# Performance work log

Hardware: AMD Instinct MI355X
Metric: run time of the kernel (lower is better)

Reference implementation:

```python
import jax, jax.numpy as jnp
import numpy as np

EPS = 1e-8

def squash(t, axis=-1):
    sq = jnp.sum(t * t, axis=axis, keepdims=True)
    scale = sq / (1.0 + sq)
    return scale * t / jnp.sqrt(sq + EPS)

def setup_inputs() -> dict:
    key = jax.random.key(0)
    k1, k2 = jax.random.split(key)
    B, N_IN, D_IN, N_OUT, D_OUT = 256, 1152, 8, 10, 16
    x = jax.random.normal(k1, (B, N_IN, D_IN), dtype=jnp.float32)
    W = 0.01 * jax.random.normal(k2, (1, N_IN, N_OUT, D_OUT, D_IN), dtype=jnp.float32)
    return {"x": x, "W": W}

def reference(x, W):
    # u_hat[b,n,o,j] = sum_i W[0,n,o,j,i] * x[b,n,i]   -> (B, N_in, N_out, D_out)
    u_hat = jnp.einsum('noji,bni->bnoj', W[0], x)
    # b_ij starts with batch dim 1 (as in original torch code) and broadcasts
    b_ij = jnp.zeros((1, u_hat.shape[1], u_hat.shape[2], 1), dtype=u_hat.dtype)
    v_j = None
    for _ in range(3):  # fixed 3 routing iterations
        c_ij = jax.nn.softmax(b_ij, axis=2)            # over output capsules
        s_j = jnp.sum(c_ij * u_hat, axis=1, keepdims=True)  # (B,1,N_out,D_out)
        v_j = squash(s_j, axis=-1)
        b_ij = b_ij + jnp.sum(u_hat * v_j, axis=-1, keepdims=True)
    return jnp.squeeze(v_j, axis=1)  # (B, N_out, D_out)
```

## Files before the change

### kernel.cpp

```cpp
#include <hip/hip_runtime.h>

#define B_ 256
#define N_IN 1152
#define N_OUT 10
#define D_OUT 16
#define OJ 160
#define SN (B_*OJ)
#define LOG2E 1.44269504088896340736f
#define NPB 16
#define NPW 4
#define NGB (N_IN/NPB)

typedef __attribute__((ext_vector_type(8))) short bf16x8;
typedef __attribute__((ext_vector_type(4))) float f32x4;

#define NW_ELEMS (N_IN*N_OUT*D_OUT)
#define NWB (NW_ELEMS/256)
#define XTB ((N_IN/16)*(B_/16))

__device__ __forceinline__ unsigned short f2bf(float f) {
  unsigned u = __float_as_uint(f);
  u += 0x7fffu + ((u >> 16) & 1u);
  return (unsigned short)(u >> 16);
}
__device__ __forceinline__ float bf2f(unsigned short s) {
  return __uint_as_float(((unsigned)s) << 16);
}

template<int CTRL>
__device__ __forceinline__ float dpp_add(float x) {
  int y = __builtin_amdgcn_mov_dpp(__float_as_int(x), CTRL, 0xF, 0xF, false);
  return x + __int_as_float(y);
}
__device__ __forceinline__ float row_sum16(float x) {
  x = dpp_add<0x128>(x); x = dpp_add<0x124>(x);
  x = dpp_add<0x122>(x); x = dpp_add<0x121>(x);
  return x;
}

__global__ __launch_bounds__(256) void pack_all(const float* __restrict__ W,
                                                const float* __restrict__ x,
                                                short* __restrict__ WH, short* __restrict__ WL,
                                                short* __restrict__ XH, short* __restrict__ XL) {
  const int bid = blockIdx.x;
  const int tid = threadIdx.x;
  if (bid < NWB) {
    const int t = bid*256 + tid;
    const float4 a = ((const float4*)W)[t*2];
    const float4 b = ((const float4*)W)[t*2+1];
    const float w[8] = {a.x,a.y,a.z,a.w,b.x,b.y,b.z,b.w};
    bf16x8 vh, vl;
#pragma unroll
    for (int e=0;e<8;e++){
      unsigned short hh = f2bf(w[e]);
      vh[e] = (short)hh;
      vl[e] = (short)f2bf(w[e] - bf2f(hh));
    }
    ((bf16x8*)WH)[t] = vh;
    ((bf16x8*)WL)[t] = vl;
  } else {
    __shared__ bf16x8 TH[16*17], TL[16*17];
    const int bid2 = bid - NWB;
    const int nt = bid2 >> 4, bt = bid2 & 15;
    const int nn = tid & 15, bb = tid >> 4;
    const size_t r = (size_t)((bt*16 + bb)*N_IN + nt*16 + nn);
    const float4 a = ((const float4*)x)[r*2];
    const float4 c = ((const float4*)x)[r*2+1];
    const float w[8] = {a.x,a.y,a.z,a.w,c.x,c.y,c.z,c.w};
    bf16x8 vh, vl;
#pragma unroll
    for (int e=0;e<8;e++){
      unsigned short hh = f2bf(w[e]);
      vh[e] = (short)hh;
      vl[e] = (short)f2bf(w[e] - bf2f(hh));
    }
    TH[nn*17 + bb] = vh;
    TL[nn*17 + bb] = vl;
    __syncthreads();
    const int bb2 = tid & 15, nn2 = tid >> 4;
    const size_t o = (size_t)(nt*16 + nn2)*B_ + bt*16 + bb2;
    ((bf16x8*)XH)[o] = TH[nn2*17 + bb2];
    ((bf16x8*)XL)[o] = TL[nn2*17 + bb2];
  }
}


__global__ __launch_bounds__(256) void pass1(const short* __restrict__ WH,
                                             const short* __restrict__ WL,
                                             const short* __restrict__ XH,
                                             const short* __restrict__ XL,
                                             float* __restrict__ P) {
  __shared__ f32x4 red[3*640];
  const int tid = threadIdx.x, w = tid >> 6, l = tid & 63;
  const int bb = l & 15, c = l >> 4;
  const int b0 = blockIdx.y * 16;
  const int n0 = blockIdx.x * NPB + w * NPW;
  const short* Abase = (c & 1)  ? WL : WH;
  const short* Bbase = (c >> 1) ? XL : XH;

  f32x4 acc[N_OUT];
  const f32x4 zz = {0.f,0.f,0.f,0.f};
#pragma unroll
  for (int o=0;o<N_OUT;o++) acc[o] = zz;

  for (int nn=0; nn<NPW; ++nn) {
    const int n = n0 + nn;
    const bf16x8 bfrag = *(const bf16x8*)&Bbase[((size_t)n*B_ + b0 + bb)*8];
    const short* Ap = &Abase[(size_t)n*1280 + bb*8];
#pragma unroll
    for (int o=0;o<N_OUT;o++) {
      const bf16x8 afrag = *(const bf16x8*)&Ap[o*128];
      acc[o] = __builtin_amdgcn_mfma_f32_16x16x32_bf16(afrag, bfrag, acc[o], 0,0,0);
    }
  }

  const int slot = bb*4 + c;
  if (w) {
    f32x4* r = &red[(w-1)*640];
#pragma unroll
    for (int o=0;o<N_OUT;o++) r[o*64 + slot] = acc[o];
  }
  __syncthreads();
  if (!w) {
#pragma unroll
    for (int o=0;o<N_OUT;o++)
      acc[o] += red[o*64+slot] + red[640+o*64+slot] + red[1280+o*64+slot];
    float* Pp = &P[((size_t)blockIdx.x*B_ + b0 + bb)*OJ + c*4];
#pragma unroll
    for (int o=0;o<N_OUT;o++) *(f32x4*)&Pp[o*16] = acc[o];
  }
}

__global__ __launch_bounds__(256) void pass23(const short* __restrict__ WH,
                                              const short* __restrict__ WL,
                                              const short* __restrict__ XH,
                                              const short* __restrict__ XL,
                                              const float* __restrict__ veff,
                                              float* __restrict__ P) {
  __shared__ f32x4 red[3*640];
  const int tid = threadIdx.x, w = tid >> 6, l = tid & 63;
  const int bb = l & 15, c = l >> 4;
  const int b0 = blockIdx.y * 16;
  const int n0 = blockIdx.x * NPB + w * NPW;
  const short* Abase = (c & 1)  ? WL : WH;
  const short* Bbase = (c >> 1) ? XL : XH;

  f32x4 vj[N_OUT], acc[N_OUT];
  const f32x4 zz = {0.f,0.f,0.f,0.f};
  const float* vp = &veff[(size_t)(b0+bb)*OJ + c*4];
#pragma unroll
  for (int o=0;o<N_OUT;o++) { vj[o] = *(const f32x4*)&vp[o*16]; acc[o] = zz; }

  for (int nn=0; nn<NPW; ++nn) {
    const int n = n0 + nn;
    const bf16x8 bfrag = *(const bf16x8*)&Bbase[((size_t)n*B_ + b0 + bb)*8];
    const short* Ap = &Abase[(size_t)n*1280 + bb*8];
    f32x4 u[N_OUT];
#pragma unroll
    for (int o=0;o<N_OUT;o++) {
      const bf16x8 afrag = *(const bf16x8*)&Ap[o*128];
      u[o] = __builtin_amdgcn_mfma_f32_16x16x32_bf16(afrag, bfrag, zz, 0,0,0);
    }
    float ez[N_OUT], Z = 0.f;
#pragma unroll
    for (int o=0;o<N_OUT;o++) {
      float t = u[o][0]*vj[o][0] + u[o][1]*vj[o][1]
              + u[o][2]*vj[o][2] + u[o][3]*vj[o][3];
      t += __shfl_xor(t, 16);
      t += __shfl_xor(t, 32);
      ez[o] = exp2f(t);
      Z += ez[o];
    }
    const float invZ = 1.f / Z;
#pragma unroll
    for (int o=0;o<N_OUT;o++) acc[o] += (ez[o] * invZ) * u[o];
  }

  const int slot = bb*4 + c;
  if (w) {
    f32x4* r = &red[(w-1)*640];
#pragma unroll
    for (int o=0;o<N_OUT;o++) r[o*64 + slot] = acc[o];
  }
  __syncthreads();
  if (!w) {
#pragma unroll
    for (int o=0;o<N_OUT;o++)
      acc[o] += red[o*64+slot] + red[640+o*64+slot] + red[1280+o*64+slot];
    float* Pp = &P[((size_t)blockIdx.x*B_ + b0 + bb)*OJ + c*4];
#pragma unroll
    for (int o=0;o<N_OUT;o++) *(f32x4*)&Pp[o*16] = acc[o];
  }
}

__global__ __launch_bounds__(256) void finish(const float* __restrict__ P, float scale,
                                              const float* __restrict__ vprev,
                                              float* __restrict__ vout, float lscale) {
  const int idx = blockIdx.x*256 + threadIdx.x;
  float t = 0.f;
#pragma unroll 8
  for (int g=0; g<NGB; ++g) t += P[(size_t)g*SN + idx];
  t *= scale;
  const float sq = row_sum16(t * t);
  float v = t * (sq / (1.f + sq)) * rsqrtf(sq + 1e-8f);
  v *= lscale;
  if (vprev != nullptr) v += vprev[idx];
  vout[idx] = v;
}

extern "C" void kernel_launch(void* const* d_in, const int* in_sizes, int n_in,
                              void* d_out, int out_size, void* d_ws, size_t ws_size,
                              hipStream_t stream) {
  const float* x = (const float*)d_in[0];
  const float* W = (const float*)d_in[1];
  float* out = (float*)d_out;

  float* P   = (float*)d_ws;
  float* v1  = P  + (size_t)NGB*SN;
  float* v12 = v1 + SN;
  short* WH = (short*)(v12 + SN);
  short* WL = WH + (size_t)NW_ELEMS*8;
  short* XH = WL + (size_t)NW_ELEMS*8;
  short* XL = XH + (size_t)(B_*N_IN)*8;

  pack_all<<<NWB + XTB, 256, 0, stream>>>(W, x, WH, WL, XH, XL);

  const dim3 pg(NGB, 16), pb(256);

  pass1<<<pg, pb, 0, stream>>>(WH, WL, XH, XL, P);
  finish<<<SN/256, 256, 0, stream>>>(P, 0.1f, nullptr, v1, LOG2E);

  pass23<<<pg, pb, 0, stream>>>(WH, WL, XH, XL, v1, P);
  finish<<<SN/256, 256, 0, stream>>>(P, 1.0f, v1, v12, LOG2E);

  pass23<<<pg, pb, 0, stream>>>(WH, WL, XH, XL, v12, P);
  finish<<<SN/256, 256, 0, stream>>>(P, 1.0f, nullptr, out, 1.0f);
}
```

Before: 88.59 us.

## Fuse packing and routing passes into a single cooperative persistent kernel

Replaces seven separate launches (pack, three passes, three finishes) with one cooperative kernel of 256 blocks × 512 threads that uses grid.sync between stages, removing launch gaps. The n-split drops from 72 groups to 16, so each block covers 72 n values with 8 waves and a tree reduction in LDS, and the finish step reads 16 partials instead of 72. A fallback launches the old multi-kernel path if the cooperative launch fails. Risks: grid-wide barrier cost, only 256 blocks for the packing stage, and less parallelism per pass.

```diff
diff --git a/kernel.cpp b/kernel.cpp
--- a/kernel.cpp
+++ b/kernel.cpp
@@ -1,22 +1,25 @@
 #include <hip/hip_runtime.h>
+#include <hip/hip_cooperative_groups.h>
+
+namespace cg = cooperative_groups;
 
 #define B_ 256
 #define N_IN 1152
 #define N_OUT 10
-#define D_OUT 16
 #define OJ 160
 #define SN (B_*OJ)
 #define LOG2E 1.44269504088896340736f
-#define NPB 16
-#define NPW 4
-#define NGB (N_IN/NPB)
+#define SGN 16
+#define NPS (N_IN/SGN)
+#define NTHR 512
+#define NBLK 256
+#define GSZ (NBLK*NTHR)
+#define NW_ELEMS (N_IN*N_OUT*16)
+#define NX_ELEMS (B_*N_IN)
+#define NTILES ((N_IN/16)*(B_/16))
 
 typedef __attribute__((ext_vector_type(8))) short bf16x8;
 typedef __attribute__((ext_vector_type(4))) float f32x4;
-
-#define NW_ELEMS (N_IN*N_OUT*D_OUT)
-#define NWB (NW_ELEMS/256)
-#define XTB ((N_IN/16)*(B_/16))
 
 __device__ __forceinline__ unsigned short f2bf(float f) {
   unsigned u = __float_as_uint(f);
@@ -26,94 +29,281 @@
 __device__ __forceinline__ float bf2f(unsigned short s) {
   return __uint_as_float(((unsigned)s) << 16);
 }
+__device__ __forceinline__ void split8(const float* p, bf16x8& vh, bf16x8& vl) {
+  const float4 a = *(const float4*)p;
+  const float4 b = *(const float4*)(p + 4);
+  const float w[8] = {a.x,a.y,a.z,a.w,b.x,b.y,b.z,b.w};
+#pragma unroll
+  for (int e=0;e<8;e++){
+    unsigned short hh = f2bf(w[e]);
+    vh[e] = (short)hh;
+    vl[e] = (short)f2bf(w[e] - bf2f(hh));
+  }
+}
 
 template<int CTRL>
-__device__ __forceinline__ float dpp_add(float x) {
-  int y = __builtin_amdgcn_mov_dpp(__float_as_int(x), CTRL, 0xF, 0xF, false);
-  return x + __int_as_float(y);
-}
-__device__ __forceinline__ float row_sum16(float x) {
-  x = dpp_add<0x128>(x); x = dpp_add<0x124>(x);
-  x = dpp_add<0x122>(x); x = dpp_add<0x121>(x);
-  return x;
-}
-
-__global__ __launch_bounds__(256) void pack_all(const float* __restrict__ W,
-                                                const float* __restrict__ x,
-                                                short* __restrict__ WH, short* __restrict__ WL,
-                                                short* __restrict__ XH, short* __restrict__ XL) {
+__device__ __forceinline__ float dpp_add(float xx) {
+  int y = __builtin_amdgcn_mov_dpp(__float_as_int(xx), CTRL, 0xF, 0xF, false);
+  return xx + __int_as_float(y);
+}
+__device__ __forceinline__ float row_sum16(float xx) {
+  xx = dpp_add<0x128>(xx); xx = dpp_add<0x124>(xx);
+  xx = dpp_add<0x122>(xx); xx = dpp_add<0x121>(xx);
+  return xx;
+}
+__device__ __forceinline__ float squash_elem(float t) {
+  const float sq = row_sum16(t * t);
+  return t * (sq / (1.f + sq)) * rsqrtf(sq + 1e-8f);
+}
+
+template<bool UNIFORM>
+__device__ __forceinline__ void pass_core(const short* __restrict__ Abase,
+                                          const short* __restrict__ Bbase,
+                                          const float* __restrict__ veff,
+                                          float* __restrict__ P,
+                                          float (*red)[2560],
+                                          int sg, int b0, int n0,
+                                          int w, int bb, int c) {
+  const f32x4 zz = {0.f,0.f,0.f,0.f};
+  f32x4 acc[N_OUT], vj[N_OUT];
+#pragma unroll
+  for (int o=0;o<N_OUT;o++) acc[o] = zz;
+  if (!UNIFORM) {
+    const float* vp = &veff[(size_t)(b0+bb)*OJ + c*4];
+#pragma unroll
+    for (int o=0;o<N_OUT;o++) vj[o] = *(const f32x4*)&vp[o*16];
+  }
+  for (int k=0;k<9;k++) {
+    const int n = n0 + w + 8*k;
+    const bf16x8 bfrag = *(const bf16x8*)&Bbase[((size_t)n*B_ + b0 + bb)*8];
+    const short* Ap = &Abase[(size_t)n*1280 + bb*8];
+    if (UNIFORM) {
+#pragma unroll
+      for (int o=0;o<N_OUT;o++) {
+        const bf16x8 afrag = *(const bf16x8*)&Ap[o*128];
+        acc[o] = __builtin_amdgcn_mfma_f32_16x16x32_bf16(afrag, bfrag, acc[o], 0,0,0);
+      }
+    } else {
+      f32x4 u[N_OUT];
+#pragma unroll
+      for (int o=0;o<N_OUT;o++) {
+        const bf16x8 afrag = *(const bf16x8*)&Ap[o*128];
+        u[o] = __builtin_amdgcn_mfma_f32_16x16x32_bf16(afrag, bfrag, zz, 0,0,0);
+      }
+      float ez[N_OUT], Z = 0.f;
+#pragma unroll
+      for (int o=0;o<N_OUT;o++) {
+        float t = u[o][0]*vj[o][0] + u[o][1]*vj[o][1]
+                + u[o][2]*vj[o][2] + u[o][3]*vj[o][3];
+        t += __shfl_xor(t, 16);
+        t += __shfl_xor(t, 32);
+        ez[o] = exp2f(t);
+        Z += ez[o];
+      }
+      const float invZ = 1.f / Z;
+#pragma unroll
+      for (int o=0;o<N_OUT;o++) acc[o] += (ez[o]*invZ) * u[o];
+    }
+  }
+  const int slot4 = (bb*4 + c)*4;
+  if (w >= 4) {
+#pragma unroll
+    for (int o=0;o<N_OUT;o++) *(f32x4*)&red[w-4][o*256 + slot4] = acc[o];
+  }
+  __syncthreads();
+  if (w < 4) {
+#pragma unroll
+    for (int o=0;o<N_OUT;o++) acc[o] += *(const f32x4*)&red[w][o*256 + slot4];
+  }
+  __syncthreads();
+  if (w == 2 || w == 3) {
+#pragma unroll
+    for (int o=0;o<N_OUT;o++) *(f32x4*)&red[w-2][o*256 + slot4] = acc[o];
+  }
+  __syncthreads();
+  if (w < 2) {
+#pragma unroll
+    for (int o=0;o<N_OUT;o++) acc[o] += *(const f32x4*)&red[w][o*256 + slot4];
+  }
+  __syncthreads();
+  if (w == 1) {
+#pragma unroll
+    for (int o=0;o<N_OUT;o++) *(f32x4*)&red[0][o*256 + slot4] = acc[o];
+  }
+  __syncthreads();
+  if (w == 0) {
+    float* Pp = &P[(size_t)sg*SN + (size_t)(b0+bb)*OJ + c*4];
+#pragma unroll
+    for (int o=0;o<N_OUT;o++) {
+      acc[o] += *(const f32x4*)&red[0][o*256 + slot4];
+      *(f32x4*)&Pp[o*16] = acc[o];
+    }
+  }
+  __syncthreads();
+}
+
+__global__ __launch_bounds__(NTHR) void caps_mega(
+    const float* __restrict__ W, const float* __restrict__ x,
+    short* __restrict__ WH, short* __restrict__ WL,
+    short* __restrict__ XH, short* __restrict__ XL,
+    float* __restrict__ P, float* __restrict__ v1buf,
+    float* __restrict__ v12buf, float* __restrict__ out) {
+  cg::grid_group grid = cg::this_grid();
+  __shared__ float red[4][2560];
+  const int tid = threadIdx.x;
   const int bid = blockIdx.x;
-  const int tid = threadIdx.x;
+  const int gtid = bid*NTHR + tid;
+
+  for (int t = gtid; t < NW_ELEMS; t += GSZ) {
+    bf16x8 vh, vl;
+    split8(W + (size_t)t*8, vh, vl);
+    ((bf16x8*)WH)[t] = vh; ((bf16x8*)WL)[t] = vl;
+  }
+  {
+    const int unit = tid >> 8, utid = tid & 255;
+    bf16x8* TH = (bf16x8*)red + unit*544;
+    bf16x8* TL = TH + 272;
+    for (int iter = 0; iter < 3; ++iter) {
+      const int tile = iter*(NBLK*2) + bid*2 + unit;
+      const bool ok = tile < NTILES;
+      int nt = 0, bt = 0;
+      if (ok) {
+        nt = tile >> 4; bt = tile & 15;
+        const int nn = utid & 15, bb = utid >> 4;
+        bf16x8 vh, vl;
+        split8(x + ((size_t)(bt*16+bb)*N_IN + nt*16+nn)*8, vh, vl);
+        TH[nn*17 + bb] = vh; TL[nn*17 + bb] = vl;
+      }
+      __syncthreads();
+      if (ok) {
+        const int bb2 = utid & 15, nn2 = utid >> 4;
+        const size_t o = (size_t)(nt*16+nn2)*B_ + bt*16 + bb2;
+        ((bf16x8*)XH)[o] = TH[nn2*17 + bb2];
+        ((bf16x8*)XL)[o] = TL[nn2*17 + bb2];
+      }
+      __syncthreads();
+    }
+  }
+  grid.sync();
+
+  const int sg = bid >> 4, bg = bid & 15;
+  const int b0 = bg*16, n0 = sg*NPS;
+  const int w = tid >> 6, l = tid & 63;
+  const int bb = l & 15, c = l >> 4;
+  const short* Abase = (c & 1)  ? WL : WH;
+  const short* Bbase = (c >> 1) ? XL : XH;
+
+  pass_core<true>(Abase, Bbase, nullptr, P, red, sg, b0, n0, w, bb, c);
+  grid.sync();
+  if (gtid < SN) {
+    float s = 0.f;
+#pragma unroll
+    for (int g=0; g<SGN; ++g) s += P[(size_t)g*SN + gtid];
+    v1buf[gtid] = squash_elem(0.1f*s) * LOG2E;
+  }
+  grid.sync();
+  pass_core<false>(Abase, Bbase, v1buf, P, red, sg, b0, n0, w, bb, c);
+  grid.sync();
+  if (gtid < SN) {
+    float s = 0.f;
+#pragma unroll
+    for (int g=0; g<SGN; ++g) s += P[(size_t)g*SN + gtid];
+    v12buf[gtid] = v1buf[gtid] + squash_elem(s) * LOG2E;
+  }
+  grid.sync();
+  pass_core<false>(Abase, Bbase, v12buf, P, red, sg, b0, n0, w, bb, c);
+  grid.sync();
+  if (gtid < SN) {
+    float s = 0.f;
+#pragma unroll
+    for (int g=0; g<SGN; ++g) s += P[(size_t)g*SN + gtid];
+    out[gtid] = squash_elem(s);
+  }
+}
+
+#define NWB (NW_ELEMS/256)
+__global__ __launch_bounds__(256) void fb_pack(const float* __restrict__ W,
+                                               const float* __restrict__ x,
+                                               short* __restrict__ WH, short* __restrict__ WL,
+                                               short* __restrict__ XH, short* __restrict__ XL) {
+  const int bid = blockIdx.x, tid = threadIdx.x;
   if (bid < NWB) {
     const int t = bid*256 + tid;
-    const float4 a = ((const float4*)W)[t*2];
-    const float4 b = ((const float4*)W)[t*2+1];
-    const float w[8] = {a.x,a.y,a.z,a.w,b.x,b.y,b.z,b.w};
-    bf16x8 vh, vl;
-#pragma unroll
-    for (int e=0;e<8;e++){
-      unsigned short hh = f2bf(w[e]);
-      vh[e] = (short)hh;
-      vl[e] = (short)f2bf(w[e] - bf2f(hh));
-    }
-    ((bf16x8*)WH)[t] = vh;
-    ((bf16x8*)WL)[t] = vl;
+    bf16x8 vh, vl; split8(W + (size_t)t*8, vh, vl);
+    ((bf16x8*)WH)[t] = vh; ((bf16x8*)WL)[t] = vl;
   } else {
     __shared__ bf16x8 TH[16*17], TL[16*17];
-    const int bid2 = bid - NWB;
-    const int nt = bid2 >> 4, bt = bid2 & 15;
+    const int tile = bid - NWB;
+    const int nt = tile >> 4, bt = tile & 15;
     const int nn = tid & 15, bb = tid >> 4;
-    const size_t r = (size_t)((bt*16 + bb)*N_IN + nt*16 + nn);
-    const float4 a = ((const float4*)x)[r*2];
-    const float4 c = ((const float4*)x)[r*2+1];
-    const float w[8] = {a.x,a.y,a.z,a.w,c.x,c.y,c.z,c.w};
     bf16x8 vh, vl;
-#pragma unroll
-    for (int e=0;e<8;e++){
-      unsigned short hh = f2bf(w[e]);
-      vh[e] = (short)hh;
-      vl[e] = (short)f2bf(w[e] - bf2f(hh));
-    }
-    TH[nn*17 + bb] = vh;
-    TL[nn*17 + bb] = vl;
+    split8(x + ((size_t)(bt*16+bb)*N_IN + nt*16+nn)*8, vh, vl);
+    TH[nn*17 + bb] = vh; TL[nn*17 + bb] = vl;
     __syncthreads();
     const int bb2 = tid & 15, nn2 = tid >> 4;
-    const size_t o = (size_t)(nt*16 + nn2)*B_ + bt*16 + bb2;
+    const size_t o = (size_t)(nt*16+nn2)*B_ + bt*16 + bb2;
     ((bf16x8*)XH)[o] = TH[nn2*17 + bb2];
     ((bf16x8*)XL)[o] = TL[nn2*17 + bb2];
   }
 }
 
-
-__global__ __launch_bounds__(256) void pass1(const short* __restrict__ WH,
-                                             const short* __restrict__ WL,
-                                             const short* __restrict__ XH,
-                                             const short* __restrict__ XL,
-                                             float* __restrict__ P) {
+template<bool UNIFORM>
+__global__ __launch_bounds__(256) void fb_pass(const short* __restrict__ WH,
+                                               const short* __restrict__ WL,
+                                               const short* __restrict__ XH,
+                                               const short* __restrict__ XL,
+                                               const float* __restrict__ veff,
+                                               float* __restrict__ P) {
   __shared__ f32x4 red[3*640];
   const int tid = threadIdx.x, w = tid >> 6, l = tid & 63;
   const int bb = l & 15, c = l >> 4;
-  const int b0 = blockIdx.y * 16;
-  const int n0 = blockIdx.x * NPB + w * NPW;
+  const int sg = blockIdx.x, bg = blockIdx.y;
+  const int b0 = bg*16;
+  const int n0 = sg*NPS + w*18;
   const short* Abase = (c & 1)  ? WL : WH;
   const short* Bbase = (c >> 1) ? XL : XH;
 
-  f32x4 acc[N_OUT];
   const f32x4 zz = {0.f,0.f,0.f,0.f};
+  f32x4 acc[N_OUT], vj[N_OUT];
 #pragma unroll
   for (int o=0;o<N_OUT;o++) acc[o] = zz;
-
-  for (int nn=0; nn<NPW; ++nn) {
+  if (!UNIFORM) {
+    const float* vp = &veff[(size_t)(b0+bb)*OJ + c*4];
+#pragma unroll
+    for (int o=0;o<N_OUT;o++) vj[o] = *(const f32x4*)&vp[o*16];
+  }
+  for (int nn=0; nn<18; ++nn) {
     const int n = n0 + nn;
     const bf16x8 bfrag = *(const bf16x8*)&Bbase[((size_t)n*B_ + b0 + bb)*8];
     const short* Ap = &Abase[(size_t)n*1280 + bb*8];
-#pragma unroll
-    for (int o=0;o<N_OUT;o++) {
-      const bf16x8 afrag = *(const bf16x8*)&Ap[o*128];
-      acc[o] = __builtin_amdgcn_mfma_f32_16x16x32_bf16(afrag, bfrag, acc[o], 0,0,0);
+    if (UNIFORM) {
+#pragma unroll
+      for (int o=0;o<N_OUT;o++) {
+        const bf16x8 afrag = *(const bf16x8*)&Ap[o*128];
+        acc[o] = __builtin_amdgcn_mfma_f32_16x16x32_bf16(afrag, bfrag, acc[o], 0,0,0);
+      }
+    } else {
+      f32x4 u[N_OUT];
+#pragma unroll
+      for (int o=0;o<N_OUT;o++) {
+        const bf16x8 afrag = *(const bf16x8*)&Ap[o*128];
+        u[o] = __builtin_amdgcn_mfma_f32_16x16x32_bf16(afrag, bfrag, zz, 0,0,0);
+      }
+      float ez[N_OUT], Z = 0.f;
+#pragma unroll
+      for (int o=0;o<N_OUT;o++) {
+        float t = u[o][0]*vj[o][0] + u[o][1]*vj[o][1]
+                + u[o][2]*vj[o][2] + u[o][3]*vj[o][3];
+        t += __shfl_xor(t, 16);
+        t += __shfl_xor(t, 32);
+        ez[o] = exp2f(t);
+        Z += ez[o];
+      }
+      const float invZ = 1.f / Z;
+#pragma unroll
+      for (int o=0;o<N_OUT;o++) acc[o] += (ez[o]*invZ)*u[o];
     }
   }
-
   const int slot = bb*4 + c;
   if (w) {
     f32x4* r = &red[(w-1)*640];
@@ -125,85 +315,21 @@
 #pragma unroll
     for (int o=0;o<N_OUT;o++)
       acc[o] += red[o*64+slot] + red[640+o*64+slot] + red[1280+o*64+slot];
-    float* Pp = &P[((size_t)blockIdx.x*B_ + b0 + bb)*OJ + c*4];
+    float* Pp = &P[(size_t)sg*SN + (size_t)(b0+bb)*OJ + c*4];
 #pragma unroll
     for (int o=0;o<N_OUT;o++) *(f32x4*)&Pp[o*16] = acc[o];
   }
 }
 
-__global__ __launch_bounds__(256) void pass23(const short* __restrict__ WH,
-                                              const short* __restrict__ WL,
-                                              const short* __restrict__ XH,
-                                              const short* __restrict__ XL,
-                                              const float* __restrict__ veff,
-                                              float* __restrict__ P) {
-  __shared__ f32x4 red[3*640];
-  const int tid = threadIdx.x, w = tid >> 6, l = tid & 63;
-  const int bb = l & 15, c = l >> 4;
-  const int b0 = blockIdx.y * 16;
-  const int n0 = blockIdx.x * NPB + w * NPW;
-  const short* Abase = (c & 1)  ? WL : WH;
-  const short* Bbase = (c >> 1) ? XL : XH;
-
-  f32x4 vj[N_OUT], acc[N_OUT];
-  const f32x4 zz = {0.f,0.f,0.f,0.f};
-  const float* vp = &veff[(size_t)(b0+bb)*OJ + c*4];
-#pragma unroll
-  for (int o=0;o<N_OUT;o++) { vj[o] = *(const f32x4*)&vp[o*16]; acc[o] = zz; }
-
-  for (int nn=0; nn<NPW; ++nn) {
-    const int n = n0 + nn;
-    const bf16x8 bfrag = *(const bf16x8*)&Bbase[((size_t)n*B_ + b0 + bb)*8];
-    const short* Ap = &Abase[(size_t)n*1280 + bb*8];
-    f32x4 u[N_OUT];
-#pragma unroll
-    for (int o=0;o<N_OUT;o++) {
-      const bf16x8 afrag = *(const bf16x8*)&Ap[o*128];
-      u[o] = __builtin_amdgcn_mfma_f32_16x16x32_bf16(afrag, bfrag, zz, 0,0,0);
-    }
-    float ez[N_OUT], Z = 0.f;
-#pragma unroll
-    for (int o=0;o<N_OUT;o++) {
-      float t = u[o][0]*vj[o][0] + u[o][1]*vj[o][1]
-              + u[o][2]*vj[o][2] + u[o][3]*vj[o][3];
-      t += __shfl_xor(t, 16);
-      t += __shfl_xor(t, 32);
-      ez[o] = exp2f(t);
-      Z += ez[o];
-    }
-    const float invZ = 1.f / Z;
-#pragma unroll
-    for (int o=0;o<N_OUT;o++) acc[o] += (ez[o] * invZ) * u[o];
-  }
-
-  const int slot = bb*4 + c;
-  if (w) {
-    f32x4* r = &red[(w-1)*640];
-#pragma unroll
-    for (int o=0;o<N_OUT;o++) r[o*64 + slot] = acc[o];
-  }
-  __syncthreads();
-  if (!w) {
-#pragma unroll
-    for (int o=0;o<N_OUT;o++)
-      acc[o] += red[o*64+slot] + red[640+o*64+slot] + red[1280+o*64+slot];
-    float* Pp = &P[((size_t)blockIdx.x*B_ + b0 + bb)*OJ + c*4];
-#pragma unroll
-    for (int o=0;o<N_OUT;o++) *(f32x4*)&Pp[o*16] = acc[o];
-  }
-}
-
-__global__ __launch_bounds__(256) void finish(const float* __restrict__ P, float scale,
-                                              const float* __restrict__ vprev,
-                                              float* __restrict__ vout, float lscale) {
+__global__ __launch_bounds__(256) void fb_finish(const float* __restrict__ P, float scale,
+                                                 const float* __restrict__ vprev,
+                                                 float* __restrict__ vout, float lscale) {
   const int idx = blockIdx.x*256 + threadIdx.x;
   float t = 0.f;
-#pragma unroll 8
-  for (int g=0; g<NGB; ++g) t += P[(size_t)g*SN + idx];
+#pragma unroll
+  for (int g=0; g<SGN; ++g) t += P[(size_t)g*SN + idx];
   t *= scale;
-  const float sq = row_sum16(t * t);
-  float v = t * (sq / (1.f + sq)) * rsqrtf(sq + 1e-8f);
-  v *= lscale;
+  float v = squash_elem(t) * lscale;
   if (vprev != nullptr) v += vprev[idx];
   vout[idx] = v;
 }
@@ -216,23 +342,25 @@
   float* out = (float*)d_out;
 
   float* P   = (float*)d_ws;
-  float* v1  = P  + (size_t)NGB*SN;
+  float* v1  = P  + (size_t)SGN*SN;
   float* v12 = v1 + SN;
   short* WH = (short*)(v12 + SN);
   short* WL = WH + (size_t)NW_ELEMS*8;
   short* XH = WL + (size_t)NW_ELEMS*8;
-  short* XL = XH + (size_t)(B_*N_IN)*8;
-
-  pack_all<<<NWB + XTB, 256, 0, stream>>>(W, x, WH, WL, XH, XL);
-
-  const dim3 pg(NGB, 16), pb(256);
-
-  pass1<<<pg, pb, 0, stream>>>(WH, WL, XH, XL, P);
-  finish<<<SN/256, 256, 0, stream>>>(P, 0.1f, nullptr, v1, LOG2E);
-
-  pass23<<<pg, pb, 0, stream>>>(WH, WL, XH, XL, v1, P);
-  finish<<<SN/256, 256, 0, stream>>>(P, 1.0f, v1, v12, LOG2E);
-
-  pass23<<<pg, pb, 0, stream>>>(WH, WL, XH, XL, v12, P);
-  finish<<<SN/256, 256, 0, stream>>>(P, 1.0f, nullptr, out, 1.0f);
-}
+  short* XL = XH + (size_t)NX_ELEMS*8;
+
+  void* args[] = {(void*)&W, (void*)&x, (void*)&WH, (void*)&WL, (void*)&XH,
+                  (void*)&XL, (void*)&P, (void*)&v1, (void*)&v12, (void*)&out};
+  hipError_t err = hipLaunchCooperativeKernel((const void*)caps_mega,
+                                              dim3(NBLK), dim3(NTHR), args, 0, stream);
+  if (err != hipSuccess) {
+    fb_pack<<<NWB + NTILES, 256, 0, stream>>>(W, x, WH, WL, XH, XL);
+    const dim3 pg(SGN, 16), pb(256);
+    fb_pass<true ><<<pg, pb, 0, stream>>>(WH, WL, XH, XL, nullptr, P);
+    fb_finish<<<SN/256, 256, 0, stream>>>(P, 0.1f, nullptr, v1, LOG2E);
+    fb_pass<false><<<pg, pb, 0, stream>>>(WH, WL, XH, XL, v1, P);
+    fb_finish<<<SN/256, 256, 0, stream>>>(P, 1.0f, v1, v12, LOG2E);
+    fb_pass<false><<<pg, pb, 0, stream>>>(WH, WL, XH, XL, v12, P);
+    fb_finish<<<SN/256, 256, 0, stream>>>(P, 1.0f, nullptr, out, 1.0f);
+  }
+}
```

Result: slower. 275.6 us (+211.1%).

## Fuse squash/finish into routing passes via last-block ticket and coarsen N split

Applied to the files above, without the earlier changes.

Removes the three separate finish kernels. The last 16 blocks of each routing pass to arrive take an atomic ticket, spin until the counter reaches the total block count, then reduce the partial sums and apply squash directly. The input-capsule split is also coarsened from 72 to 48 groups, so each block handles 24 capsules. This shrinks the partial-sum buffer and the reduction work. The cost is spin-waiting by a few blocks, less parallelism in the reduction tail, and per-pass counters that pack_all must reset.

```diff
diff --git a/kernel.cpp b/kernel.cpp
--- a/kernel.cpp
+++ b/kernel.cpp
@@ -3,20 +3,23 @@
 #define B_ 256
 #define N_IN 1152
 #define N_OUT 10
-#define D_OUT 16
 #define OJ 160
 #define SN (B_*OJ)
 #define LOG2E 1.44269504088896340736f
-#define NPB 16
-#define NPW 4
-#define NGB (N_IN/NPB)
+#define NSG 48
+#define NPB (N_IN/NSG)
+#define NPW (NPB/4)
+#define TOTB (NSG*16)
+#define FINB 16
+#define SLICE (SN/FINB)
 
 typedef __attribute__((ext_vector_type(8))) short bf16x8;
 typedef __attribute__((ext_vector_type(4))) float f32x4;
 
-#define NW_ELEMS (N_IN*N_OUT*D_OUT)
+#define NW_ELEMS (N_IN*N_OUT*16)
+#define NX_ELEMS (B_*N_IN)
 #define NWB (NW_ELEMS/256)
-#define XTB ((N_IN/16)*(B_/16))
+#define NTILES ((N_IN/16)*(B_/16))
 
 __device__ __forceinline__ unsigned short f2bf(float f) {
   unsigned u = __float_as_uint(f);
@@ -26,186 +29,162 @@
 __device__ __forceinline__ float bf2f(unsigned short s) {
   return __uint_as_float(((unsigned)s) << 16);
 }
+__device__ __forceinline__ void split8(const float* p, bf16x8& vh, bf16x8& vl) {
+  const float4 a = *(const float4*)p;
+  const float4 b = *(const float4*)(p + 4);
+  const float w[8] = {a.x,a.y,a.z,a.w,b.x,b.y,b.z,b.w};
+#pragma unroll
+  for (int e=0;e<8;e++){
+    unsigned short hh = f2bf(w[e]);
+    vh[e] = (short)hh;
+    vl[e] = (short)f2bf(w[e] - bf2f(hh));
+  }
+}
 
 template<int CTRL>
-__device__ __forceinline__ float dpp_add(float x) {
-  int y = __builtin_amdgcn_mov_dpp(__float_as_int(x), CTRL, 0xF, 0xF, false);
-  return x + __int_as_float(y);
-}
-__device__ __forceinline__ float row_sum16(float x) {
-  x = dpp_add<0x128>(x); x = dpp_add<0x124>(x);
-  x = dpp_add<0x122>(x); x = dpp_add<0x121>(x);
-  return x;
+__device__ __forceinline__ float dpp_add(float xx) {
+  int y = __builtin_amdgcn_mov_dpp(__float_as_int(xx), CTRL, 0xF, 0xF, false);
+  return xx + __int_as_float(y);
+}
+__device__ __forceinline__ float row_sum16(float xx) {
+  xx = dpp_add<0x128>(xx); xx = dpp_add<0x124>(xx);
+  xx = dpp_add<0x122>(xx); xx = dpp_add<0x121>(xx);
+  return xx;
+}
+__device__ __forceinline__ float squash_elem(float t) {
+  const float sq = row_sum16(t * t);
+  return t * (sq / (1.f + sq)) * rsqrtf(sq + 1e-8f);
 }
 
 __global__ __launch_bounds__(256) void pack_all(const float* __restrict__ W,
                                                 const float* __restrict__ x,
                                                 short* __restrict__ WH, short* __restrict__ WL,
-                                                short* __restrict__ XH, short* __restrict__ XL) {
-  const int bid = blockIdx.x;
-  const int tid = threadIdx.x;
+                                                short* __restrict__ XH, short* __restrict__ XL,
+                                                int* __restrict__ cnt) {
+  const int bid = blockIdx.x, tid = threadIdx.x;
+  if (bid == 0 && tid < 48) cnt[tid] = 0;
   if (bid < NWB) {
     const int t = bid*256 + tid;
-    const float4 a = ((const float4*)W)[t*2];
-    const float4 b = ((const float4*)W)[t*2+1];
-    const float w[8] = {a.x,a.y,a.z,a.w,b.x,b.y,b.z,b.w};
-    bf16x8 vh, vl;
-#pragma unroll
-    for (int e=0;e<8;e++){
-      unsigned short hh = f2bf(w[e]);
-      vh[e] = (short)hh;
-      vl[e] = (short)f2bf(w[e] - bf2f(hh));
-    }
-    ((bf16x8*)WH)[t] = vh;
-    ((bf16x8*)WL)[t] = vl;
+    bf16x8 vh, vl; split8(W + (size_t)t*8, vh, vl);
+    ((bf16x8*)WH)[t] = vh; ((bf16x8*)WL)[t] = vl;
   } else {
     __shared__ bf16x8 TH[16*17], TL[16*17];
-    const int bid2 = bid - NWB;
-    const int nt = bid2 >> 4, bt = bid2 & 15;
+    const int tile = bid - NWB;
+    const int nt = tile >> 4, bt = tile & 15;
     const int nn = tid & 15, bb = tid >> 4;
-    const size_t r = (size_t)((bt*16 + bb)*N_IN + nt*16 + nn);
-    const float4 a = ((const float4*)x)[r*2];
-    const float4 c = ((const float4*)x)[r*2+1];
-    const float w[8] = {a.x,a.y,a.z,a.w,c.x,c.y,c.z,c.w};
     bf16x8 vh, vl;
-#pragma unroll
-    for (int e=0;e<8;e++){
-      unsigned short hh = f2bf(w[e]);
-      vh[e] = (short)hh;
-      vl[e] = (short)f2bf(w[e] - bf2f(hh));
-    }
-    TH[nn*17 + bb] = vh;
-    TL[nn*17 + bb] = vl;
+    split8(x + ((size_t)(bt*16+bb)*N_IN + nt*16+nn)*8, vh, vl);
+    TH[nn*17 + bb] = vh; TL[nn*17 + bb] = vl;
     __syncthreads();
     const int bb2 = tid & 15, nn2 = tid >> 4;
-    const size_t o = (size_t)(nt*16 + nn2)*B_ + bt*16 + bb2;
+    const size_t o = (size_t)(nt*16+nn2)*B_ + bt*16 + bb2;
     ((bf16x8*)XH)[o] = TH[nn2*17 + bb2];
     ((bf16x8*)XL)[o] = TL[nn2*17 + bb2];
   }
 }
 
-
-__global__ __launch_bounds__(256) void pass1(const short* __restrict__ WH,
-                                             const short* __restrict__ WL,
-                                             const short* __restrict__ XH,
-                                             const short* __restrict__ XL,
-                                             float* __restrict__ P) {
+template<int MODE>
+__global__ __launch_bounds__(256) void caps_pass(
+    const short* __restrict__ WH, const short* __restrict__ WL,
+    const short* __restrict__ XH, const short* __restrict__ XL,
+    const float* __restrict__ veff, float* __restrict__ P,
+    const float* __restrict__ vprev, float* __restrict__ vout,
+    int* __restrict__ cnt) {
   __shared__ f32x4 red[3*640];
+  __shared__ int ticket_s;
   const int tid = threadIdx.x, w = tid >> 6, l = tid & 63;
   const int bb = l & 15, c = l >> 4;
-  const int b0 = blockIdx.y * 16;
-  const int n0 = blockIdx.x * NPB + w * NPW;
+  const int sg = blockIdx.x, bg = blockIdx.y;
+  const int b0 = bg*16;
+  const int n0 = sg*NPB + w*NPW;
   const short* Abase = (c & 1)  ? WL : WH;
   const short* Bbase = (c >> 1) ? XL : XH;
 
-  f32x4 acc[N_OUT];
   const f32x4 zz = {0.f,0.f,0.f,0.f};
+  f32x4 acc[N_OUT], vj[N_OUT];
 #pragma unroll
   for (int o=0;o<N_OUT;o++) acc[o] = zz;
+  if (MODE != 0) {
+    const float* vp = &veff[(size_t)(b0+bb)*OJ + c*4];
+#pragma unroll
+    for (int o=0;o<N_OUT;o++) vj[o] = *(const f32x4*)&vp[o*16];
+  }
 
   for (int nn=0; nn<NPW; ++nn) {
     const int n = n0 + nn;
     const bf16x8 bfrag = *(const bf16x8*)&Bbase[((size_t)n*B_ + b0 + bb)*8];
     const short* Ap = &Abase[(size_t)n*1280 + bb*8];
-#pragma unroll
-    for (int o=0;o<N_OUT;o++) {
-      const bf16x8 afrag = *(const bf16x8*)&Ap[o*128];
-      acc[o] = __builtin_amdgcn_mfma_f32_16x16x32_bf16(afrag, bfrag, acc[o], 0,0,0);
+    if (MODE == 0) {
+#pragma unroll
+      for (int o=0;o<N_OUT;o++) {
+        const bf16x8 afrag = *(const bf16x8*)&Ap[o*128];
+        acc[o] = __builtin_amdgcn_mfma_f32_16x16x32_bf16(afrag, bfrag, acc[o], 0,0,0);
+      }
+    } else {
+      f32x4 u[N_OUT];
+#pragma unroll
+      for (int o=0;o<N_OUT;o++) {
+        const bf16x8 afrag = *(const bf16x8*)&Ap[o*128];
+        u[o] = __builtin_amdgcn_mfma_f32_16x16x32_bf16(afrag, bfrag, zz, 0,0,0);
+      }
+      float ez[N_OUT], Z = 0.f;
+#pragma unroll
+      for (int o=0;o<N_OUT;o++) {
+        float t = u[o][0]*vj[o][0] + u[o][1]*vj[o][1]
+                + u[o][2]*vj[o][2] + u[o][3]*vj[o][3];
+        t += __shfl_xor(t, 16);
+        t += __shfl_xor(t, 32);
+        ez[o] = exp2f(t);
+        Z += ez[o];
+      }
+      const float invZ = 1.f / Z;
+#pragma unroll
+      for (int o=0;o<N_OUT;o++) acc[o] += (ez[o]*invZ) * u[o];
     }
   }
 
-  const int slot = bb*4 + c;
   if (w) {
-    f32x4* r = &red[(w-1)*640];
-#pragma unroll
-    for (int o=0;o<N_OUT;o++) r[o*64 + slot] = acc[o];
+#pragma unroll
+    for (int o=0;o<N_OUT;o++) red[(w-1)*640 + o*64 + l] = acc[o];
   }
   __syncthreads();
   if (!w) {
 #pragma unroll
     for (int o=0;o<N_OUT;o++)
-      acc[o] += red[o*64+slot] + red[640+o*64+slot] + red[1280+o*64+slot];
-    float* Pp = &P[((size_t)blockIdx.x*B_ + b0 + bb)*OJ + c*4];
+      acc[o] += red[o*64+l] + red[640+o*64+l] + red[1280+o*64+l];
+    float* Pp = &P[(size_t)sg*SN + (size_t)(b0+bb)*OJ + c*4];
 #pragma unroll
     for (int o=0;o<N_OUT;o++) *(f32x4*)&Pp[o*16] = acc[o];
   }
-}
-
-__global__ __launch_bounds__(256) void pass23(const short* __restrict__ WH,
-                                              const short* __restrict__ WL,
-                                              const short* __restrict__ XH,
-                                              const short* __restrict__ XL,
-                                              const float* __restrict__ veff,
-                                              float* __restrict__ P) {
-  __shared__ f32x4 red[3*640];
-  const int tid = threadIdx.x, w = tid >> 6, l = tid & 63;
-  const int bb = l & 15, c = l >> 4;
-  const int b0 = blockIdx.y * 16;
-  const int n0 = blockIdx.x * NPB + w * NPW;
-  const short* Abase = (c & 1)  ? WL : WH;
-  const short* Bbase = (c >> 1) ? XL : XH;
-
-  f32x4 vj[N_OUT], acc[N_OUT];
-  const f32x4 zz = {0.f,0.f,0.f,0.f};
-  const float* vp = &veff[(size_t)(b0+bb)*OJ + c*4];
-#pragma unroll
-  for (int o=0;o<N_OUT;o++) { vj[o] = *(const f32x4*)&vp[o*16]; acc[o] = zz; }
-
-  for (int nn=0; nn<NPW; ++nn) {
-    const int n = n0 + nn;
-    const bf16x8 bfrag = *(const bf16x8*)&Bbase[((size_t)n*B_ + b0 + bb)*8];
-    const short* Ap = &Abase[(size_t)n*1280 + bb*8];
-    f32x4 u[N_OUT];
-#pragma unroll
-    for (int o=0;o<N_OUT;o++) {
-      const bf16x8 afrag = *(const bf16x8*)&Ap[o*128];
-      u[o] = __builtin_amdgcn_mfma_f32_16x16x32_bf16(afrag, bfrag, zz, 0,0,0);
-    }
-    float ez[N_OUT], Z = 0.f;
-#pragma unroll
-    for (int o=0;o<N_OUT;o++) {
-      float t = u[o][0]*vj[o][0] + u[o][1]*vj[o][1]
-              + u[o][2]*vj[o][2] + u[o][3]*vj[o][3];
-      t += __shfl_xor(t, 16);
-      t += __shfl_xor(t, 32);
-      ez[o] = exp2f(t);
-      Z += ez[o];
-    }
-    const float invZ = 1.f / Z;
-#pragma unroll
-    for (int o=0;o<N_OUT;o++) acc[o] += (ez[o] * invZ) * u[o];
-  }
-
-  const int slot = bb*4 + c;
-  if (w) {
-    f32x4* r = &red[(w-1)*640];
-#pragma unroll
-    for (int o=0;o<N_OUT;o++) r[o*64 + slot] = acc[o];
-  }
+
+  __threadfence();
+  if (tid == 0) ticket_s = atomicAdd(cnt, 1);
   __syncthreads();
-  if (!w) {
-#pragma unroll
-    for (int o=0;o<N_OUT;o++)
-      acc[o] += red[o*64+slot] + red[640+o*64+slot] + red[1280+o*64+slot];
-    float* Pp = &P[((size_t)blockIdx.x*B_ + b0 + bb)*OJ + c*4];
-#pragma unroll
-    for (int o=0;o<N_OUT;o++) *(f32x4*)&Pp[o*16] = acc[o];
-  }
-}
-
-__global__ __launch_bounds__(256) void finish(const float* __restrict__ P, float scale,
-                                              const float* __restrict__ vprev,
-                                              float* __restrict__ vout, float lscale) {
-  const int idx = blockIdx.x*256 + threadIdx.x;
-  float t = 0.f;
-#pragma unroll 8
-  for (int g=0; g<NGB; ++g) t += P[(size_t)g*SN + idx];
-  t *= scale;
-  const float sq = row_sum16(t * t);
-  float v = t * (sq / (1.f + sq)) * rsqrtf(sq + 1e-8f);
-  v *= lscale;
-  if (vprev != nullptr) v += vprev[idx];
-  vout[idx] = v;
+  const int rank = ticket_s - (TOTB - FINB);
+  if (rank < 0 || rank >= FINB) return;
+  if (tid == 0) {
+    while (__hip_atomic_load(cnt, __ATOMIC_ACQUIRE, __HIP_MEMORY_SCOPE_AGENT) < TOTB)
+      __builtin_amdgcn_s_sleep(2);
+  }
+  __syncthreads();
+  __threadfence();
+
+  const int base = rank*SLICE + tid;
+  float s[10];
+#pragma unroll
+  for (int e=0;e<10;e++) s[e] = 0.f;
+  for (int g=0; g<NSG; ++g) {
+    const float* Pg = &P[(size_t)g*SN + base];
+#pragma unroll
+    for (int e=0;e<10;e++) s[e] += Pg[256*e];
+  }
+#pragma unroll
+  for (int e=0;e<10;e++) {
+    float t = s[e] * (MODE == 0 ? 0.1f : 1.f);
+    float v = squash_elem(t) * (MODE == 2 ? 1.f : LOG2E);
+    if (MODE == 1) v += vprev[base + 256*e];
+    vout[base + 256*e] = v;
+  }
 }
 
 extern "C" void kernel_launch(void* const* d_in, const int* in_sizes, int n_in,
@@ -216,23 +195,18 @@
   float* out = (float*)d_out;
 
   float* P   = (float*)d_ws;
-  float* v1  = P  + (size_t)NGB*SN;
+  float* v1  = P  + (size_t)NSG*SN;
   float* v12 = v1 + SN;
-  short* WH = (short*)(v12 + SN);
+  int*  cnt  = (int*)(v12 + SN);
+  short* WH = (short*)(cnt + 64);
   short* WL = WH + (size_t)NW_ELEMS*8;
   short* XH = WL + (size_t)NW_ELEMS*8;
-  short* XL = XH + (size_t)(B_*N_IN)*8;
-
-  pack_all<<<NWB + XTB, 256, 0, stream>>>(W, x, WH, WL, XH, XL);
-
-  const dim3 pg(NGB, 16), pb(256);
-
-  pass1<<<pg, pb, 0, stream>>>(WH, WL, XH, XL, P);
-  finish<<<SN/256, 256, 0, stream>>>(P, 0.1f, nullptr, v1, LOG2E);
-
-  pass23<<<pg, pb, 0, stream>>>(WH, WL, XH, XL, v1, P);
-  finish<<<SN/256, 256, 0, stream>>>(P, 1.0f, v1, v12, LOG2E);
-
-  pass23<<<pg, pb, 0, stream>>>(WH, WL, XH, XL, v12, P);
-  finish<<<SN/256, 256, 0, stream>>>(P, 1.0f, nullptr, out, 1.0f);
-}
+  short* XL = XH + (size_t)NX_ELEMS*8;
+
+  pack_all<<<NWB + NTILES, 256, 0, stream>>>(W, x, WH, WL, XH, XL, cnt);
+
+  const dim3 pg(NSG, 16), pb(256);
+  caps_pass<0><<<pg, pb, 0, stream>>>(WH, WL, XH, XL, nullptr, P, nullptr, v1,  cnt);
+  caps_pass<1><<<pg, pb, 0, stream>>>(WH, WL, XH, XL, v1,      P, v1,      v12, cnt + 16);
+  caps_pass<2><<<pg, pb, 0, stream>>>(WH, WL, XH, XL, v12,     P, nullptr, out, cnt + 32);
+}
```

Measured after the change: 347.6 us. 3.92x slower.
